# Optimization experiments

Measured on AMD Instinct MI355X. Metric: run time of the kernel, lower is better.

Reference implementation:

```python
import jax, jax.numpy as jnp
import numpy as np

N_NODES = 100000
N_EDGES = 1600000
IN_DIM = 128
OUT_DIM = 128


def setup_inputs() -> dict:
    key = jax.random.key(0)
    k1, k2, k3, k4, k5 = jax.random.split(key, 5)
    h = jax.random.normal(k1, (N_NODES, IN_DIM), dtype=jnp.float32)
    # nn.Linear(in_dim, out_dim): W [out, in], b [out]
    W = jax.random.normal(k2, (OUT_DIM, IN_DIM), dtype=jnp.float32) * (1.0 / np.sqrt(IN_DIM))
    b = jax.random.normal(k3, (OUT_DIM,), dtype=jnp.float32) * 0.01
    edge_src = jax.random.randint(k4, (N_EDGES,), 0, N_NODES, dtype=jnp.int32)
    edge_dst = jax.random.randint(k5, (N_EDGES,), 0, N_NODES, dtype=jnp.int32)
    return {"h": h, "W": W, "b": b, "edge_src": edge_src, "edge_dst": edge_dst}


def reference(h, W, b, edge_src, edge_dst):
    n = h.shape[0]
    # in-degree of each node (edges point src -> dst), clamped to >= 1
    deg = jax.ops.segment_sum(jnp.ones_like(edge_dst, dtype=h.dtype), edge_dst, num_segments=n)
    norm = jnp.power(jnp.clip(deg, 1.0), -0.5)[:, None]  # [N, 1]
    hn = h * norm
    # copy_u + sum: gather source features, scatter-add to destinations (SpMM)
    agg = jax.ops.segment_sum(hn[edge_src], edge_dst, num_segments=n)  # [N, in_dim]
    out = (agg * norm) @ W.T + b
    return out
```

## Files before the change

### kernel.cpp

```cpp
#include <hip/hip_runtime.h>
#include <hip/hip_fp16.h>

#define DIM 128
#define TSH 8
#define TSZ 256
#define EBLK 4096

typedef _Float16 half8_t __attribute__((ext_vector_type(8)));
typedef float f32x4 __attribute__((ext_vector_type(4)));
typedef float f32x4v __attribute__((ext_vector_type(4)));


__global__ __launch_bounds__(256) void hist_a(const int* __restrict__ dst,
                                              int* __restrict__ gh,
                                              int ne, int nblk, int nt) {
    __shared__ int h[512];
    int t = threadIdx.x;
    h[t] = 0; h[t + 256] = 0;
    __syncthreads();
    int i0 = blockIdx.x * EBLK + t;
#pragma unroll
    for (int u = 0; u < 16; ++u) {
        int i = i0 + u * 256;
        if (i < ne) atomicAdd(&h[dst[i] >> TSH], 1);
    }
    __syncthreads();
    for (int k = t; k < nt; k += 256) gh[k * nblk + blockIdx.x] = h[k];
}

__global__ __launch_bounds__(256) void scan_a(int* __restrict__ g,
                                              int* __restrict__ bsum, int M) {
    __shared__ int wsum[4];
    int t = threadIdx.x;
    int base = blockIdx.x * 1024 + t * 4;
    int4 v;
    if (base + 3 < M) v = *(const int4*)(g + base);
    else {
        v.x = (base + 0 < M) ? g[base + 0] : 0;
        v.y = (base + 1 < M) ? g[base + 1] : 0;
        v.z = (base + 2 < M) ? g[base + 2] : 0;
        v.w = (base + 3 < M) ? g[base + 3] : 0;
    }
    int s3 = v.x + v.y + v.z + v.w;
    int lane = t & 63, wv = t >> 6;
    int x = s3;
#pragma unroll
    for (int off = 1; off < 64; off <<= 1) {
        int y = __shfl_up(x, off, 64);
        if (lane >= off) x += y;
    }
    if (lane == 63) wsum[wv] = x;
    __syncthreads();
    int woff = 0;
    for (int i = 0; i < wv; ++i) woff += wsum[i];
    int ex = woff + x - s3;
    int4 o;
    o.x = ex; o.y = ex + v.x; o.z = o.y + v.y; o.w = o.z + v.z;
    if (base + 3 < M) *(int4*)(g + base) = o;
    else {
        if (base + 0 < M) g[base + 0] = o.x;
        if (base + 1 < M) g[base + 1] = o.y;
        if (base + 2 < M) g[base + 2] = o.z;
        if (base + 3 < M) g[base + 3] = o.w;
    }
    if (t == 0) bsum[blockIdx.x] = wsum[0] + wsum[1] + wsum[2] + wsum[3];
}

__global__ __launch_bounds__(256) void scanb_wprep(int* __restrict__ bsum, int nb,
                                                   const float* __restrict__ W,
                                                   _Float16* __restrict__ Wf) {
    if (blockIdx.x == 0) {
        __shared__ int s[256];
        int t = threadIdx.x;
        int d = (t < nb) ? bsum[t] : 0;
        s[t] = d;
        __syncthreads();
        for (int off = 1; off < 256; off <<= 1) {
            int v = (t >= off) ? s[t - off] : 0;
            __syncthreads();
            s[t] += v;
            __syncthreads();
        }
        if (t < nb) bsum[t] = s[t] - d;
    } else {
        int idx = (blockIdx.x - 1) * 256 + threadIdx.x;
        int tile = idx >> 8;
        int kk = (idx >> 6) & 3;
        int lane = idx & 63;
        int nn = lane & 15, quad = lane >> 4;
        const float* wr = W + (tile * 16 + nn) * DIM + kk * 32 + quad * 8;
        _Float16* o = Wf + (size_t)idx * 8;
#pragma unroll
        for (int j = 0; j < 8; ++j) o[j] = (_Float16)wr[j];
    }
}

__global__ __launch_bounds__(256) void scatter_b(const int* __restrict__ src,
                                                 const int* __restrict__ dst,
                                                 const int* __restrict__ gh,
                                                 const int* __restrict__ gb,
                                                 unsigned* __restrict__ tbuf,
                                                 int ne, int nblk, int M, int nt) {
    __shared__ int h[512];
    __shared__ int ps[512];
    __shared__ int cur[512];
    __shared__ unsigned sval[EBLK];
    __shared__ unsigned short skey[EBLK];
    int t = threadIdx.x;
    int blk = blockIdx.x;

    int p0a[2];
#pragma unroll
    for (int u = 0; u < 2; ++u) {
        int k = t + u * 256;
        int c = 0, p0 = 0;
        if (k < nt) {
            int idx = k * nblk + blk;
            p0 = gh[idx] + gb[idx >> 10];
            int p1 = (idx + 1 < M) ? (gh[idx + 1] + gb[(idx + 1) >> 10]) : ne;
            c = p1 - p0;
        }
        h[k] = c;
        p0a[u] = p0;
    }
    __syncthreads();
    int h0 = h[2 * t];
    int s2 = h0 + h[2 * t + 1];
    ps[t] = s2;
    __syncthreads();
    for (int off = 1; off < 256; off <<= 1) {
        int v = (t >= off) ? ps[t - off] : 0;
        __syncthreads();
        ps[t] += v;
        __syncthreads();
    }
    int inc = ps[t];
    __syncthreads();
    int ex0 = inc - s2;
    ps[2 * t] = ex0;
    ps[2 * t + 1] = ex0 + h0;
    cur[2 * t] = ex0;
    cur[2 * t + 1] = ex0 + h0;
    __syncthreads();
#pragma unroll
    for (int u = 0; u < 2; ++u) {
        int k = t + u * 256;
        h[k] = p0a[u] - ps[k];
    }
    __syncthreads();

    int i0 = blk * EBLK + t;
#pragma unroll
    for (int u = 0; u < 16; ++u) {
        int i = i0 + u * 256;
        if (i < ne) {
            int d = dst[i];
            int key = d >> TSH;
            int r = atomicAdd(&cur[key], 1);
            sval[r] = ((unsigned)src[i] << TSH) | (unsigned)(d & (TSZ - 1));
            skey[r] = (unsigned short)key;
        }
    }
    __syncthreads();
    int cnt = ne - blk * EBLK;
    if (cnt > EBLK) cnt = EBLK;
    for (int p = t; p < cnt; p += 256)
        tbuf[h[skey[p]] + p] = sval[p];
}

__global__ __launch_bounds__(256) void tile_sort(const unsigned* __restrict__ tbuf,
                                                 const int* __restrict__ gh,
                                                 const int* __restrict__ gb,
                                                 int* __restrict__ ebuf,
                                                 int* __restrict__ row_start,
                                                 int n, int ne, int nblk, int nt) {
    __shared__ int hist[TSZ];
    __shared__ int cur[TSZ];
    __shared__ int ps[TSZ];
    int t = threadIdx.x;
    int tile = blockIdx.x;
    int i0 = tile * nblk;
    int ts = gh[i0] + gb[i0 >> 10];
    int i1 = (tile + 1) * nblk;
    int te = (tile + 1 < nt) ? gh[i1] + gb[i1 >> 10] : ne;
    hist[t] = 0;
    __syncthreads();
    for (int i = ts + t; i < te; i += 256)
        atomicAdd(&hist[tbuf[i] & (TSZ - 1)], 1);
    __syncthreads();
    int d = hist[t];
    ps[t] = d;
    __syncthreads();
    for (int off = 1; off < 256; off <<= 1) {
        int v = (t >= off) ? ps[t - off] : 0;
        __syncthreads();
        ps[t] += v;
        __syncthreads();
    }
    int ex = ps[t] - d;
    cur[t] = ex;
    int node = tile * TSZ + t;
    if (node <= n) row_start[node] = ts + ex;
    __syncthreads();
    for (int i = ts + t; i < te; i += 256) {
        unsigned p = tbuf[i];
        int dl = (int)(p & (TSZ - 1));
        int r = atomicAdd(&cur[dl], 1);
        ebuf[ts + r] = (int)(p >> TSH);
    }
}

__global__ __launch_bounds__(256) void hn_pack(const float* __restrict__ h,
                                               const int* __restrict__ rs,
                                               float2* __restrict__ hn, int n32) {
    int i = blockIdx.x * 256 + threadIdx.x;
    if (i >= n32) return;
    int node = i >> 5;
    int d = rs[node + 1] - rs[node];
    float sc = rsqrtf((float)(d > 1 ? d : 1));
    f32x4v v = __builtin_nontemporal_load((const f32x4v*)h + i);
    union { __half2 h2[2]; float2 f2; } u;
    u.h2[0] = __floats2half2_rn(v.x * sc, v.y * sc);
    u.h2[1] = __floats2half2_rn(v.z * sc, v.w * sc);
    hn[i] = u.f2;
}

__global__ __launch_bounds__(512) void gather_gemm(const float2* __restrict__ hn,
                                                   const int* __restrict__ ebuf,
                                                   const int* __restrict__ rs,
                                                   const _Float16* __restrict__ Wf,
                                                   const float* __restrict__ b,
                                                   float* __restrict__ out, int n) {
    __shared__ _Float16 xs[64 * 136];
    int tid = threadIdx.x;
    int g = tid >> 5, lane = tid & 31;

#pragma unroll
    for (int it = 0; it < 4; ++it) {
        int row = it * 16 + g;
        int node = blockIdx.x * 64 + row;
        union { __half2 h2[2]; float2 f2; } u;
        if (node < n) {
            int s0 = rs[node];
            int s1 = rs[node + 1];
            __half2 a0 = __floats2half2_rn(0.f, 0.f), a1 = a0;
            int i = s0;
            for (; i + 7 < s1; i += 8) {
                int e0 = ebuf[i], e1 = ebuf[i + 1], e2 = ebuf[i + 2], e3 = ebuf[i + 3];
                int e4 = ebuf[i + 4], e5 = ebuf[i + 5], e6 = ebuf[i + 6], e7 = ebuf[i + 7];
                float2 r0 = hn[(size_t)e0 * 32 + lane];
                float2 r1 = hn[(size_t)e1 * 32 + lane];
                float2 r2 = hn[(size_t)e2 * 32 + lane];
                float2 r3 = hn[(size_t)e3 * 32 + lane];
                float2 r4 = hn[(size_t)e4 * 32 + lane];
                float2 r5 = hn[(size_t)e5 * 32 + lane];
                float2 r6 = hn[(size_t)e6 * 32 + lane];
                float2 r7 = hn[(size_t)e7 * 32 + lane];
                const __half2* q0 = (const __half2*)&r0;
                const __half2* q1 = (const __half2*)&r1;
                const __half2* q2 = (const __half2*)&r2;
                const __half2* q3 = (const __half2*)&r3;
                const __half2* q4 = (const __half2*)&r4;
                const __half2* q5 = (const __half2*)&r5;
                const __half2* q6 = (const __half2*)&r6;
                const __half2* q7 = (const __half2*)&r7;
                a0 = __hadd2(a0, q0[0]); a1 = __hadd2(a1, q0[1]);
                a0 = __hadd2(a0, q1[0]); a1 = __hadd2(a1, q1[1]);
                a0 = __hadd2(a0, q2[0]); a1 = __hadd2(a1, q2[1]);
                a0 = __hadd2(a0, q3[0]); a1 = __hadd2(a1, q3[1]);
                a0 = __hadd2(a0, q4[0]); a1 = __hadd2(a1, q4[1]);
                a0 = __hadd2(a0, q5[0]); a1 = __hadd2(a1, q5[1]);
                a0 = __hadd2(a0, q6[0]); a1 = __hadd2(a1, q6[1]);
                a0 = __hadd2(a0, q7[0]); a1 = __hadd2(a1, q7[1]);
            }
            for (; i + 3 < s1; i += 4) {
                int e0 = ebuf[i], e1 = ebuf[i + 1], e2 = ebuf[i + 2], e3 = ebuf[i + 3];
                float2 r0 = hn[(size_t)e0 * 32 + lane];
                float2 r1 = hn[(size_t)e1 * 32 + lane];
                float2 r2 = hn[(size_t)e2 * 32 + lane];
                float2 r3 = hn[(size_t)e3 * 32 + lane];
                const __half2* q0 = (const __half2*)&r0;
                const __half2* q1 = (const __half2*)&r1;
                const __half2* q2 = (const __half2*)&r2;
                const __half2* q3 = (const __half2*)&r3;
                a0 = __hadd2(a0, q0[0]); a1 = __hadd2(a1, q0[1]);
                a0 = __hadd2(a0, q1[0]); a1 = __hadd2(a1, q1[1]);
                a0 = __hadd2(a0, q2[0]); a1 = __hadd2(a1, q2[1]);
                a0 = __hadd2(a0, q3[0]); a1 = __hadd2(a1, q3[1]);
            }
            for (; i < s1; ++i) {
                int e0 = ebuf[i];
                float2 r0 = hn[(size_t)e0 * 32 + lane];
                const __half2* q0 = (const __half2*)&r0;
                a0 = __hadd2(a0, q0[0]); a1 = __hadd2(a1, q0[1]);
            }
            int dn = s1 - s0;
            float nd = rsqrtf((float)(dn > 1 ? dn : 1));
            float2 f0 = __half22float2(a0), f1 = __half22float2(a1);
            u.h2[0] = __floats2half2_rn(f0.x * nd, f0.y * nd);
            u.h2[1] = __floats2half2_rn(f1.x * nd, f1.y * nd);
        } else {
            u.h2[0] = __floats2half2_rn(0.f, 0.f);
            u.h2[1] = u.h2[0];
        }
        *(float2*)(xs + row * 136 + lane * 4) = u.f2;
    }
    __syncthreads();

    int w = tid >> 6;
    int wl = tid & 63;
    int cn = wl & 15;
    int quad = wl >> 4;

    f32x4 acc[4] = {{0.f, 0.f, 0.f, 0.f}, {0.f, 0.f, 0.f, 0.f},
                    {0.f, 0.f, 0.f, 0.f}, {0.f, 0.f, 0.f, 0.f}};
#pragma unroll
    for (int kk = 0; kk < 4; ++kk) {
        half8_t bf = ((const half8_t*)Wf)[(w * 4 + kk) * 64 + wl];
#pragma unroll
        for (int rt = 0; rt < 4; ++rt) {
            half8_t af = *(const half8_t*)(xs + (rt * 16 + cn) * 136 + kk * 32 + quad * 8);
            acc[rt] = __builtin_amdgcn_mfma_f32_16x16x32_f16(af, bf, acc[rt], 0, 0, 0);
        }
    }
    float bj = b[w * 16 + cn];
    int node0 = blockIdx.x * 64;
#pragma unroll
    for (int rt = 0; rt < 4; ++rt) {
#pragma unroll
        for (int r = 0; r < 4; ++r) {
            int node = node0 + rt * 16 + quad * 4 + r;
            if (node < n)
                __builtin_nontemporal_store(acc[rt][r] + bj,
                                            &out[(size_t)node * DIM + w * 16 + cn]);
        }
    }
}

extern "C" void kernel_launch(void* const* d_in, const int* in_sizes, int n_in,
                              void* d_out, int out_size, void* d_ws, size_t ws_size,
                              hipStream_t stream) {
    const float* h = (const float*)d_in[0];
    const float* W = (const float*)d_in[1];
    const float* b = (const float*)d_in[2];
    const int* esrc = (const int*)d_in[3];
    const int* edst = (const int*)d_in[4];
    float* out = (float*)d_out;

    int n = in_sizes[0] / DIM;
    int ne = in_sizes[3];

    int nblk = (ne + EBLK - 1) / EBLK;
    int nt = (n + TSZ - 1) >> TSH;
    int M = nt * nblk;
    int nsc = (M + 1023) / 1024;

    float2* hn = (float2*)d_ws;
    _Float16* Wf = (_Float16*)(hn + (size_t)n * 32);
    int* row_start = (int*)(Wf + 16384);
    int* gh = row_start + (n + 1);
    int* gbsum = gh + M;
    unsigned* tbuf = (unsigned*)(gbsum + 256);
    int* ebuf = (int*)(tbuf + ne);

    hist_a<<<nblk, 256, 0, stream>>>(edst, gh, ne, nblk, nt);
    scan_a<<<nsc, 256, 0, stream>>>(gh, gbsum, M);
    scanb_wprep<<<9, 256, 0, stream>>>(gbsum, nsc, W, Wf);
    scatter_b<<<nblk, 256, 0, stream>>>(esrc, edst, gh, gbsum, tbuf, ne, nblk, M, nt);
    tile_sort<<<nt, 256, 0, stream>>>(tbuf, gh, gbsum, ebuf, row_start, n, ne, nblk, nt);
    hn_pack<<<(n * 32 + 255) / 256, 256, 0, stream>>>(h, row_start, hn, n * 32);
    gather_gemm<<<(n + 63) / 64, 512, 0, stream>>>(hn, ebuf, row_start, Wf, b, out, n);
}
```

Before: 228.1 us.

## Fuse preprocessing kernels and widen blocks to 1024 threads

Merges the W-to-fp16 prep into hist_a, and removes the separate block-sum scan kernel by having scatter_b and tile_sort each redo the small block-sum scan in shared memory. Folds hn_pack into tile_sort, taking the degree scale straight from the per-tile histogram. All preprocessing kernels move to 1024-thread blocks. This cuts two launches and one pass over row_start, at the cost of repeating the block-sum scan in every block and a larger, less occupancy-friendly tile_sort that now also streams h.

```diff
diff --git a/kernel.cpp b/kernel.cpp
--- a/kernel.cpp
+++ b/kernel.cpp
@@ -11,21 +11,36 @@
 typedef float f32x4v __attribute__((ext_vector_type(4)));
 
 
-__global__ __launch_bounds__(256) void hist_a(const int* __restrict__ dst,
-                                              int* __restrict__ gh,
-                                              int ne, int nblk, int nt) {
+__global__ __launch_bounds__(1024) void hist_a(const int* __restrict__ dst,
+                                               int* __restrict__ gh,
+                                               int ne, int nblk, int nt,
+                                               const float* __restrict__ W,
+                                               _Float16* __restrict__ Wf) {
     __shared__ int h[512];
     int t = threadIdx.x;
-    h[t] = 0; h[t + 256] = 0;
-    __syncthreads();
-    int i0 = blockIdx.x * EBLK + t;
-#pragma unroll
-    for (int u = 0; u < 16; ++u) {
-        int i = i0 + u * 256;
+    int blk = blockIdx.x;
+    if (blk >= nblk) {
+        int idx = (blk - nblk) * 1024 + t;
+        int tile = idx >> 8;
+        int kk = (idx >> 6) & 3;
+        int lane = idx & 63;
+        int nn = lane & 15, quad = lane >> 4;
+        const float* wr = W + (tile * 16 + nn) * DIM + kk * 32 + quad * 8;
+        _Float16* o = Wf + (size_t)idx * 8;
+#pragma unroll
+        for (int j = 0; j < 8; ++j) o[j] = (_Float16)wr[j];
+        return;
+    }
+    if (t < 512) h[t] = 0;
+    __syncthreads();
+    int i0 = blk * EBLK + t;
+#pragma unroll
+    for (int u = 0; u < 4; ++u) {
+        int i = i0 + u * 1024;
         if (i < ne) atomicAdd(&h[dst[i] >> TSH], 1);
     }
     __syncthreads();
-    for (int k = t; k < nt; k += 256) gh[k * nblk + blockIdx.x] = h[k];
+    for (int k = t; k < nt; k += 1024) gh[k * nblk + blk] = h[k];
 }
 
 __global__ __launch_bounds__(256) void scan_a(int* __restrict__ g,
@@ -66,93 +81,66 @@
     if (t == 0) bsum[blockIdx.x] = wsum[0] + wsum[1] + wsum[2] + wsum[3];
 }
 
-__global__ __launch_bounds__(256) void scanb_wprep(int* __restrict__ bsum, int nb,
-                                                   const float* __restrict__ W,
-                                                   _Float16* __restrict__ Wf) {
-    if (blockIdx.x == 0) {
-        __shared__ int s[256];
-        int t = threadIdx.x;
-        int d = (t < nb) ? bsum[t] : 0;
-        s[t] = d;
-        __syncthreads();
-        for (int off = 1; off < 256; off <<= 1) {
-            int v = (t >= off) ? s[t - off] : 0;
-            __syncthreads();
-            s[t] += v;
-            __syncthreads();
-        }
-        if (t < nb) bsum[t] = s[t] - d;
-    } else {
-        int idx = (blockIdx.x - 1) * 256 + threadIdx.x;
-        int tile = idx >> 8;
-        int kk = (idx >> 6) & 3;
-        int lane = idx & 63;
-        int nn = lane & 15, quad = lane >> 4;
-        const float* wr = W + (tile * 16 + nn) * DIM + kk * 32 + quad * 8;
-        _Float16* o = Wf + (size_t)idx * 8;
-#pragma unroll
-        for (int j = 0; j < 8; ++j) o[j] = (_Float16)wr[j];
-    }
-}
-
-__global__ __launch_bounds__(256) void scatter_b(const int* __restrict__ src,
-                                                 const int* __restrict__ dst,
-                                                 const int* __restrict__ gh,
-                                                 const int* __restrict__ gb,
-                                                 unsigned* __restrict__ tbuf,
-                                                 int ne, int nblk, int M, int nt) {
-    __shared__ int h[512];
-    __shared__ int ps[512];
+__global__ __launch_bounds__(1024) void scatter_b(const int* __restrict__ src,
+                                                  const int* __restrict__ dst,
+                                                  const int* __restrict__ gh,
+                                                  const int* __restrict__ bsum,
+                                                  unsigned* __restrict__ tbuf,
+                                                  int ne, int nblk, int M, int nt,
+                                                  int nsc) {
+    __shared__ int hD[512];
+    __shared__ int ps[256];
     __shared__ int cur[512];
+    __shared__ int gbl[256];
     __shared__ unsigned sval[EBLK];
     __shared__ unsigned short skey[EBLK];
-    int t = threadIdx.x;
-    int blk = blockIdx.x;
-
-    int p0a[2];
-#pragma unroll
-    for (int u = 0; u < 2; ++u) {
-        int k = t + u * 256;
-        int c = 0, p0 = 0;
-        if (k < nt) {
-            int idx = k * nblk + blk;
-            p0 = gh[idx] + gb[idx >> 10];
-            int p1 = (idx + 1 < M) ? (gh[idx + 1] + gb[(idx + 1) >> 10]) : ne;
+    int t = threadIdx.x, blk = blockIdx.x;
+
+    int bd = 0;
+    if (t < 256) { bd = (t < nsc) ? bsum[t] : 0; ps[t] = bd; }
+    __syncthreads();
+    for (int off = 1; off < 256; off <<= 1) {
+        int v = (t < 256 && t >= off) ? ps[t - off] : 0;
+        __syncthreads();
+        if (t < 256) ps[t] += v;
+        __syncthreads();
+    }
+    if (t < 256) gbl[t] = ps[t] - bd;
+    __syncthreads();
+
+    int p0 = 0, c = 0;
+    if (t < 512) {
+        if (t < nt) {
+            int idx = t * nblk + blk;
+            p0 = gh[idx] + gbl[idx >> 10];
+            int p1 = (idx + 1 < M) ? (gh[idx + 1] + gbl[(idx + 1) >> 10]) : ne;
             c = p1 - p0;
         }
-        h[k] = c;
-        p0a[u] = p0;
-    }
-    __syncthreads();
-    int h0 = h[2 * t];
-    int s2 = h0 + h[2 * t + 1];
-    ps[t] = s2;
+        hD[t] = c;
+    }
+    __syncthreads();
+    int h0 = 0, h1 = 0;
+    if (t < 256) { h0 = hD[2 * t]; h1 = hD[2 * t + 1]; ps[t] = h0 + h1; }
     __syncthreads();
     for (int off = 1; off < 256; off <<= 1) {
-        int v = (t >= off) ? ps[t - off] : 0;
-        __syncthreads();
-        ps[t] += v;
-        __syncthreads();
-    }
-    int inc = ps[t];
-    __syncthreads();
-    int ex0 = inc - s2;
-    ps[2 * t] = ex0;
-    ps[2 * t + 1] = ex0 + h0;
-    cur[2 * t] = ex0;
-    cur[2 * t + 1] = ex0 + h0;
-    __syncthreads();
-#pragma unroll
-    for (int u = 0; u < 2; ++u) {
-        int k = t + u * 256;
-        h[k] = p0a[u] - ps[k];
-    }
+        int v = (t < 256 && t >= off) ? ps[t - off] : 0;
+        __syncthreads();
+        if (t < 256) ps[t] += v;
+        __syncthreads();
+    }
+    if (t < 256) {
+        int ex0 = ps[t] - h0 - h1;
+        cur[2 * t] = ex0;
+        cur[2 * t + 1] = ex0 + h0;
+    }
+    __syncthreads();
+    if (t < 512) hD[t] = p0 - cur[t];
     __syncthreads();
 
     int i0 = blk * EBLK + t;
 #pragma unroll
-    for (int u = 0; u < 16; ++u) {
-        int i = i0 + u * 256;
+    for (int u = 0; u < 4; ++u) {
+        int i = i0 + u * 1024;
         if (i < ne) {
             int d = dst[i];
             int key = d >> TSH;
@@ -164,65 +152,82 @@
     __syncthreads();
     int cnt = ne - blk * EBLK;
     if (cnt > EBLK) cnt = EBLK;
-    for (int p = t; p < cnt; p += 256)
-        tbuf[h[skey[p]] + p] = sval[p];
-}
-
-__global__ __launch_bounds__(256) void tile_sort(const unsigned* __restrict__ tbuf,
-                                                 const int* __restrict__ gh,
-                                                 const int* __restrict__ gb,
-                                                 int* __restrict__ ebuf,
-                                                 int* __restrict__ row_start,
-                                                 int n, int ne, int nblk, int nt) {
+    for (int p = t; p < cnt; p += 1024)
+        tbuf[hD[skey[p]] + p] = sval[p];
+}
+
+__global__ __launch_bounds__(1024) void tile_sort(const unsigned* __restrict__ tbuf,
+                                                  const int* __restrict__ gh,
+                                                  const int* __restrict__ bsum,
+                                                  int* __restrict__ ebuf,
+                                                  int* __restrict__ row_start,
+                                                  const float* __restrict__ hsrc,
+                                                  float2* __restrict__ hn,
+                                                  int n, int ne, int nblk, int nt,
+                                                  int nsc) {
     __shared__ int hist[TSZ];
     __shared__ int cur[TSZ];
-    __shared__ int ps[TSZ];
+    __shared__ int ps[256];
+    __shared__ int gbl[256];
+    __shared__ float scl[TSZ];
     int t = threadIdx.x;
     int tile = blockIdx.x;
+
+    int bd = 0;
+    if (t < 256) { bd = (t < nsc) ? bsum[t] : 0; ps[t] = bd; hist[t] = 0; }
+    __syncthreads();
+    for (int off = 1; off < 256; off <<= 1) {
+        int v = (t < 256 && t >= off) ? ps[t - off] : 0;
+        __syncthreads();
+        if (t < 256) ps[t] += v;
+        __syncthreads();
+    }
+    if (t < 256) gbl[t] = ps[t] - bd;
+    __syncthreads();
+
     int i0 = tile * nblk;
-    int ts = gh[i0] + gb[i0 >> 10];
+    int ts = gh[i0] + gbl[i0 >> 10];
     int i1 = (tile + 1) * nblk;
-    int te = (tile + 1 < nt) ? gh[i1] + gb[i1 >> 10] : ne;
-    hist[t] = 0;
-    __syncthreads();
-    for (int i = ts + t; i < te; i += 256)
+    int te = (tile + 1 < nt) ? gh[i1] + gbl[i1 >> 10] : ne;
+
+    for (int i = ts + t; i < te; i += 1024)
         atomicAdd(&hist[tbuf[i] & (TSZ - 1)], 1);
     __syncthreads();
-    int d = hist[t];
-    ps[t] = d;
+    int d = 0;
+    if (t < 256) { d = hist[t]; ps[t] = d; }
     __syncthreads();
     for (int off = 1; off < 256; off <<= 1) {
-        int v = (t >= off) ? ps[t - off] : 0;
-        __syncthreads();
-        ps[t] += v;
-        __syncthreads();
-    }
-    int ex = ps[t] - d;
-    cur[t] = ex;
-    int node = tile * TSZ + t;
-    if (node <= n) row_start[node] = ts + ex;
-    __syncthreads();
-    for (int i = ts + t; i < te; i += 256) {
+        int v = (t < 256 && t >= off) ? ps[t - off] : 0;
+        __syncthreads();
+        if (t < 256) ps[t] += v;
+        __syncthreads();
+    }
+    if (t < 256) {
+        int ex = ps[t] - d;
+        cur[t] = ex;
+        int node = tile * TSZ + t;
+        if (node <= n) row_start[node] = ts + ex;
+        scl[t] = rsqrtf((float)(d > 1 ? d : 1));
+    }
+    __syncthreads();
+    for (int i = ts + t; i < te; i += 1024) {
         unsigned p = tbuf[i];
         int dl = (int)(p & (TSZ - 1));
         int r = atomicAdd(&cur[dl], 1);
         ebuf[ts + r] = (int)(p >> TSH);
     }
-}
-
-__global__ __launch_bounds__(256) void hn_pack(const float* __restrict__ h,
-                                               const int* __restrict__ rs,
-                                               float2* __restrict__ hn, int n32) {
-    int i = blockIdx.x * 256 + threadIdx.x;
-    if (i >= n32) return;
-    int node = i >> 5;
-    int d = rs[node + 1] - rs[node];
-    float sc = rsqrtf((float)(d > 1 ? d : 1));
-    f32x4v v = __builtin_nontemporal_load((const f32x4v*)h + i);
-    union { __half2 h2[2]; float2 f2; } u;
-    u.h2[0] = __floats2half2_rn(v.x * sc, v.y * sc);
-    u.h2[1] = __floats2half2_rn(v.z * sc, v.w * sc);
-    hn[i] = u.f2;
+    int qbase = tile * 8192;
+    for (int q = t; q < 8192; q += 1024) {
+        int node = tile * TSZ + (q >> 5);
+        if (node < n) {
+            f32x4v v = __builtin_nontemporal_load((const f32x4v*)hsrc + qbase + q);
+            float sc = scl[q >> 5];
+            union { __half2 h2[2]; float2 f2; } u;
+            u.h2[0] = __floats2half2_rn(v.x * sc, v.y * sc);
+            u.h2[1] = __floats2half2_rn(v.z * sc, v.w * sc);
+            hn[qbase + q] = u.f2;
+        }
+    }
 }
 
 __global__ __launch_bounds__(512) void gather_gemm(const float2* __restrict__ hn,
@@ -363,11 +368,9 @@
     unsigned* tbuf = (unsigned*)(gbsum + 256);
     int* ebuf = (int*)(tbuf + ne);
 
-    hist_a<<<nblk, 256, 0, stream>>>(edst, gh, ne, nblk, nt);
+    hist_a<<<nblk + 2, 1024, 0, stream>>>(edst, gh, ne, nblk, nt, W, Wf);
     scan_a<<<nsc, 256, 0, stream>>>(gh, gbsum, M);
-    scanb_wprep<<<9, 256, 0, stream>>>(gbsum, nsc, W, Wf);
-    scatter_b<<<nblk, 256, 0, stream>>>(esrc, edst, gh, gbsum, tbuf, ne, nblk, M, nt);
-    tile_sort<<<nt, 256, 0, stream>>>(tbuf, gh, gbsum, ebuf, row_start, n, ne, nblk, nt);
-    hn_pack<<<(n * 32 + 255) / 256, 256, 0, stream>>>(h, row_start, hn, n * 32);
+    scatter_b<<<nblk, 1024, 0, stream>>>(esrc, edst, gh, gbsum, tbuf, ne, nblk, M, nt, nsc);
+    tile_sort<<<nt, 1024, 0, stream>>>(tbuf, gh, gbsum, ebuf, row_start, h, hn, n, ne, nblk, nt, nsc);
     gather_gemm<<<(n + 63) / 64, 512, 0, stream>>>(hn, ebuf, row_start, Wf, b, out, n);
 }
```

Result: faster. 216.4 us (-5.1%).
